# Performance work log

Measured on AMD Instinct MI355X. Metric: run time of the kernel, lower is better.

## Reference

```python
import jax, jax.numpy as jnp
import numpy as np

TEMP = 13.544
EPS = 1e-5  # BatchNorm2d default eps


def setup_inputs() -> dict:
    key = jax.random.key(0)
    k1, = jax.random.split(key, 1)
    N, S, E = 16, 1024, 512
    x = jax.random.normal(k1, (N, S, E), dtype=jnp.float32)
    gamma = jnp.ones((1,), dtype=jnp.float32)   # BatchNorm2d(1).weight
    beta = jnp.zeros((1,), dtype=jnp.float32)   # BatchNorm2d(1).bias
    return {"x": x, "gamma": gamma, "beta": beta}


def reference(x, gamma, beta):
    # Pairwise squared L2 distances via GEMM identity:
    # ||a-b||^2 = ||a||^2 + ||b||^2 - 2 a.b   (symmetric, matches the
    # original broadcast diff+square+sum without the O(S^2 E) intermediate)
    sq = jnp.sum(x * x, axis=-1)                    # (N, S)
    gram = jnp.einsum('bse,bte->bst', x, x)         # (N, S, S)
    d = sq[:, :, None] + sq[:, None, :] - 2.0 * gram  # (N, S, S)
    d = jnp.maximum(d, 0.0)                          # numerical floor (exact math is >= 0)

    # BatchNorm2d(1) in training mode: stats over all elements of the single channel
    d = d[:, None, :, :]                             # (N, 1, S, S)
    mean = jnp.mean(d)
    var = jnp.mean((d - mean) ** 2)                  # biased variance, as torch uses for normalization
    d_hat = (d - mean) * jax.lax.rsqrt(var + EPS)
    out = d_hat * gamma.reshape(1, 1, 1, 1) + beta.reshape(1, 1, 1, 1)

    # softmax(-out / 13.544) over last dim
    return jax.nn.softmax(-out / TEMP, axis=-1)      # (N, 1, S, S)
```

## Files before the change

kernel.cpp:

```cpp
#include <hip/hip_runtime.h>
#include <hip/hip_bf16.h>


#define S_DIM 1024
#define E_DIM 512
#define NBATCH 16
#define NSTEP (E_DIM / 32)
#define TEMP_C 13.544

typedef __attribute__((ext_vector_type(4))) float f32x4;
typedef __attribute__((ext_vector_type(8))) short bf16x8;
typedef __attribute__((ext_vector_type(8))) _Float16 f16x8;

__device__ inline unsigned pkbf(float lo, float hi) {
  unsigned a = __float_as_uint(lo), b = __float_as_uint(hi);
  a = (a + 0x7FFFu + ((a >> 16) & 1u)) >> 16;
  b = (b + 0x7FFFu + ((b >> 16) & 1u)) & 0xFFFF0000u;
  return b | a;
}

__device__ inline void gload16(const void* g, void* l) {
  __builtin_amdgcn_global_load_lds(
      (const __attribute__((address_space(1))) unsigned*)g,
      (__attribute__((address_space(3))) unsigned*)l, 16, 0, 0);
}

__global__ __launch_bounds__(256) void sqcvt(const float* __restrict__ x,
                                             ushort* __restrict__ xb16,
                                             float* __restrict__ sq,
                                             double* __restrict__ sums) {
  const int wave = threadIdx.x >> 6, lane = threadIdx.x & 63;
  const size_t row = (size_t)blockIdx.x * 4 + wave;
  const float4* xr = reinterpret_cast<const float4*>(x + row * E_DIM);
  float4 a = xr[lane * 2], b = xr[lane * 2 + 1];
  uint4 p;
  p.x = pkbf(a.x, a.y); p.y = pkbf(a.z, a.w);
  p.z = pkbf(b.x, b.y); p.w = pkbf(b.z, b.w);
  *reinterpret_cast<uint4*>(xb16 + row * E_DIM + lane * 8) = p;
  float s = a.x*a.x + a.y*a.y + a.z*a.z + a.w*a.w +
            b.x*b.x + b.y*b.y + b.z*b.z + b.w*b.w;
#pragma unroll
  for (int o = 32; o > 0; o >>= 1) s += __shfl_xor(s, o);
  if (lane == 0) sq[row] = s;
  if (blockIdx.x == 0 && threadIdx.x == 0) { sums[0] = 0.0; sums[1] = 0.0; }
}

template <int MODE>
__global__ __launch_bounds__(256) void gram4(const ushort* __restrict__ xb16,
                                             const float* __restrict__ sq,
                                             float* __restrict__ dout,
                                             _Float16* __restrict__ dp,
                                             double* __restrict__ sums) {
  __shared__ ushort lA[3][4096];
  __shared__ ushort lB[3][4096];
  __shared__ double red[8];

  const int tid = threadIdx.x, wave = tid >> 6, lane = tid & 63;
  const int wr = wave >> 1, wc = wave & 1;

  const int bid = blockIdx.x;
  const int xcd = bid & 7, li = bid >> 3;
  const int b = (xcd << 1) | (li >> 6);
  const int tile = li & 63;
  const int tr = tile >> 3, tc = tile & 7;

  const ushort* xb = xb16 + (size_t)b * (S_DIM * E_DIM);
  const int rowA0 = tr * 128, rowB0 = tc * 128;

  int eA[2], eB[2];
  const int o0 = wave * 1024 + lane * 16;
#pragma unroll
  for (int i = 0; i < 2; ++i) {
    int o = o0 + i * 4096;
    int so = o ^ (((o >> 7) & 3) << 4);
    int row = so >> 6, cb = (so >> 4) & 3;
    eA[i] = (rowA0 + row) * E_DIM + cb * 8;
    eB[i] = (rowB0 + row) * E_DIM + cb * 8;
  }

  auto stage = [&](int buf, int k0) {
    char* la = (char*)&lA[buf][0];
    char* lb = (char*)&lB[buf][0];
    gload16(xb + eA[0] + k0, la + wave * 1024);
    gload16(xb + eA[1] + k0, la + 4096 + wave * 1024);
    gload16(xb + eB[0] + k0, lb + wave * 1024);
    gload16(xb + eB[1] + k0, lb + 4096 + wave * 1024);
  };

  f32x4 acc[4][4] = {};

  stage(0, 0);
  stage(1, 32);
  int cur = 0;
#pragma unroll 1
  for (int ks = 0; ks < NSTEP; ++ks) {
    if (ks < NSTEP - 1) {
      asm volatile("s_waitcnt vmcnt(4)" ::: "memory");
    } else {
      asm volatile("s_waitcnt vmcnt(0)" ::: "memory");
    }
    __builtin_amdgcn_s_barrier();
    __builtin_amdgcn_sched_barrier(0);
    if (ks + 2 < NSTEP) {
      int nb = cur + 2; if (nb >= 3) nb -= 3;
      stage(nb, (ks + 2) * 32);
    }
    __builtin_amdgcn_sched_barrier(0);

    bf16x8 af[4], bfr[4];
    const int cb = lane >> 4;
    const char* la = (const char*)&lA[cur][0];
    const char* lb = (const char*)&lB[cur][0];
#pragma unroll
    for (int m = 0; m < 4; ++m) {
      int row = wr * 64 + m * 16 + (lane & 15);
      af[m] = *reinterpret_cast<const bf16x8*>(la + row * 64 + ((cb ^ ((row >> 1) & 3)) << 4));
    }
#pragma unroll
    for (int n = 0; n < 4; ++n) {
      int row = wc * 64 + n * 16 + (lane & 15);
      bfr[n] = *reinterpret_cast<const bf16x8*>(lb + row * 64 + ((cb ^ ((row >> 1) & 3)) << 4));
    }
#pragma unroll
    for (int m = 0; m < 4; ++m)
#pragma unroll
      for (int n = 0; n < 4; ++n)
        acc[m][n] = __builtin_amdgcn_mfma_f32_16x16x32_bf16(af[m], bfr[n], acc[m][n], 0, 0, 0);

    if (++cur >= 3) cur = 0;
  }

  const float* sqb = sq + b * S_DIM;
  double sd = 0.0, sd2 = 0.0;
#pragma unroll
  for (int m = 0; m < 4; ++m) {
    int gr0 = tr * 128 + wr * 64 + m * 16 + ((lane >> 4) << 2);
    float sqr0 = sqb[gr0], sqr1 = sqb[gr0 + 1], sqr2 = sqb[gr0 + 2], sqr3 = sqb[gr0 + 3];
#pragma unroll
    for (int n = 0; n < 4; ++n) {
      int gc = tc * 128 + wc * 64 + n * 16 + (lane & 15);
      float sqc = sqb[gc];
      float d0 = fmaxf(sqr0 + sqc - 2.0f * acc[m][n][0], 0.0f);
      float d1 = fmaxf(sqr1 + sqc - 2.0f * acc[m][n][1], 0.0f);
      float d2 = fmaxf(sqr2 + sqc - 2.0f * acc[m][n][2], 0.0f);
      float d3 = fmaxf(sqr3 + sqc - 2.0f * acc[m][n][3], 0.0f);
      if (MODE == 0) {
        float* dbase = dout + (size_t)b * S_DIM * S_DIM;
        dbase[(size_t)(gr0 + 0) * S_DIM + gc] = d0;
        dbase[(size_t)(gr0 + 1) * S_DIM + gc] = d1;
        dbase[(size_t)(gr0 + 2) * S_DIM + gc] = d2;
        dbase[(size_t)(gr0 + 3) * S_DIM + gc] = d3;
      } else {
        _Float16* dbase = dp + (size_t)b * S_DIM * S_DIM;
        dbase[(size_t)(gr0 + 0) * S_DIM + gc] = (_Float16)(d0 - sqr0);
        dbase[(size_t)(gr0 + 1) * S_DIM + gc] = (_Float16)(d1 - sqr1);
        dbase[(size_t)(gr0 + 2) * S_DIM + gc] = (_Float16)(d2 - sqr2);
        dbase[(size_t)(gr0 + 3) * S_DIM + gc] = (_Float16)(d3 - sqr3);
      }
      sd += (double)d0 + (double)d1 + (double)d2 + (double)d3;
      sd2 += (double)d0 * d0 + (double)d1 * d1 + (double)d2 * d2 + (double)d3 * d3;
    }
  }
#pragma unroll
  for (int o = 32; o > 0; o >>= 1) {
    sd += __shfl_xor(sd, o);
    sd2 += __shfl_xor(sd2, o);
  }
  if (lane == 0) { red[wave] = sd; red[4 + wave] = sd2; }
  __syncthreads();
  if (tid == 0) {
    atomicAdd(&sums[0], red[0] + red[1] + red[2] + red[3]);
    atomicAdd(&sums[1], red[4] + red[5] + red[6] + red[7]);
  }
}

__device__ inline float ln_scale(const double* sums, const float* gamma) {
  constexpr double invN = 1.0 / (16.0 * 1024.0 * 1024.0);
  double mean = sums[0] * invN;
  double var = sums[1] * invN - mean * mean;
  return (float)(-((double)gamma[0]) / (sqrt(var + 1e-5) * TEMP_C));
}

__global__ __launch_bounds__(256) void softmax_f32(float* __restrict__ d,
                                                   const double* __restrict__ sums,
                                                   const float* __restrict__ gamma) {
  const int wave = threadIdx.x >> 6, lane = threadIdx.x & 63;
  const size_t row = (size_t)blockIdx.x * 4 + wave;
  const float scale = ln_scale(sums, gamma);
  float4* r4 = reinterpret_cast<float4*>(d + row * S_DIM);
  float4 v[4];
#pragma unroll
  for (int i = 0; i < 4; ++i) v[i] = r4[lane + 64 * i];
  float l[16];
#pragma unroll
  for (int i = 0; i < 4; ++i) {
    l[4*i+0] = scale * v[i].x; l[4*i+1] = scale * v[i].y;
    l[4*i+2] = scale * v[i].z; l[4*i+3] = scale * v[i].w;
  }
  float mx = l[0];
#pragma unroll
  for (int i = 1; i < 16; ++i) mx = fmaxf(mx, l[i]);
#pragma unroll
  for (int o = 32; o > 0; o >>= 1) mx = fmaxf(mx, __shfl_xor(mx, o));
  const float L2E = 1.4426950408889634f;
  float e[16], s = 0.f;
#pragma unroll
  for (int i = 0; i < 16; ++i) { e[i] = exp2f((l[i] - mx) * L2E); s += e[i]; }
#pragma unroll
  for (int o = 32; o > 0; o >>= 1) s += __shfl_xor(s, o);
  float inv = 1.0f / s;
#pragma unroll
  for (int i = 0; i < 4; ++i)
    r4[lane + 64 * i] = make_float4(e[4*i]*inv, e[4*i+1]*inv, e[4*i+2]*inv, e[4*i+3]*inv);
}

__global__ __launch_bounds__(256) void softmax_f16(const _Float16* __restrict__ dp,
                                                   float* __restrict__ out,
                                                   const double* __restrict__ sums,
                                                   const float* __restrict__ gamma) {
  const int wave = threadIdx.x >> 6, lane = threadIdx.x & 63;
  const size_t row = (size_t)blockIdx.x * 4 + wave;
  const float scale = ln_scale(sums, gamma);
  const f16x8* r8 = reinterpret_cast<const f16x8*>(dp + row * S_DIM);
  f16x8 h0 = r8[lane * 2], h1 = r8[lane * 2 + 1];
  float l[16];
#pragma unroll
  for (int i = 0; i < 8; ++i) { l[i] = scale * (float)h0[i]; l[8 + i] = scale * (float)h1[i]; }
  float mx = l[0];
#pragma unroll
  for (int i = 1; i < 16; ++i) mx = fmaxf(mx, l[i]);
#pragma unroll
  for (int o = 32; o > 0; o >>= 1) mx = fmaxf(mx, __shfl_xor(mx, o));
  const float L2E = 1.4426950408889634f;
  float e[16], s = 0.f;
#pragma unroll
  for (int i = 0; i < 16; ++i) { e[i] = exp2f((l[i] - mx) * L2E); s += e[i]; }
#pragma unroll
  for (int o = 32; o > 0; o >>= 1) s += __shfl_xor(s, o);
  float inv = 1.0f / s;
  float4* o4 = reinterpret_cast<float4*>(out + row * S_DIM);
#pragma unroll
  for (int i = 0; i < 4; ++i)
    o4[lane * 4 + i] = make_float4(e[4*i]*inv, e[4*i+1]*inv, e[4*i+2]*inv, e[4*i+3]*inv);
}

extern "C" void kernel_launch(void* const* d_in, const int* in_sizes, int n_in,
                              void* d_out, int out_size, void* d_ws, size_t ws_size,
                              hipStream_t stream) {
  const float* x = (const float*)d_in[0];
  const float* gamma = (const float*)d_in[1];
  float* out = (float*)d_out;
  double* sums = (double*)d_ws;
  float* sq = (float*)((char*)d_ws + 256);
  ushort* xb16 = (ushort*)((char*)d_ws + 256 + 65536);
  _Float16* dp = (_Float16*)((char*)d_ws + 256 + 65536 +
                             (size_t)NBATCH * S_DIM * E_DIM * 2);
  const size_t need_b = 256 + 65536 + (size_t)NBATCH * S_DIM * E_DIM * 2;
  const size_t need_a = need_b + (size_t)NBATCH * S_DIM * S_DIM * 2;

  sqcvt<<<dim3(NBATCH * S_DIM / 4), dim3(256), 0, stream>>>(x, xb16, sq, sums);
  if (ws_size >= need_a) {
    gram4<1><<<dim3(NBATCH * 64), dim3(256), 0, stream>>>(xb16, sq, out, dp, sums);
    softmax_f16<<<dim3(NBATCH * S_DIM / 4), dim3(256), 0, stream>>>(dp, out, sums, gamma);
  } else {
    gram4<0><<<dim3(NBATCH * 64), dim3(256), 0, stream>>>(xb16, sq, out, dp, sums);
    softmax_f32<<<dim3(NBATCH * S_DIM / 4), dim3(256), 0, stream>>>(out, sums, gamma);
  }
}
```

Before: 158.7 us.

## Enlarge gram tiles to 256x256 with 8-wave blocks

The gram kernel now computes 256x256 output tiles per block using 512 threads (8 waves, 2x4 layout, each wave 128x64), instead of 128x128 tiles with 4 waves. The grid shrinks to 256 blocks, exactly one wave of blocks across the GPU, and each LDS-staged k-slice is reused across more output, which cuts global and LDS traffic per FLOP. In exchange, accumulator register use doubles, the 3-stage LDS buffers double to 96KB per block, and the reduction covers 8 waves.

```diff
diff --git a/kernel.cpp b/kernel.cpp
--- a/kernel.cpp
+++ b/kernel.cpp
@@ -46,48 +46,47 @@
 }
 
 template <int MODE>
-__global__ __launch_bounds__(256) void gram4(const ushort* __restrict__ xb16,
-                                             const float* __restrict__ sq,
-                                             float* __restrict__ dout,
-                                             _Float16* __restrict__ dp,
-                                             double* __restrict__ sums) {
-  __shared__ ushort lA[3][4096];
-  __shared__ ushort lB[3][4096];
-  __shared__ double red[8];
+__global__ __launch_bounds__(512, 2) void gram5(const ushort* __restrict__ xb16,
+                                                const float* __restrict__ sq,
+                                                float* __restrict__ dout,
+                                                _Float16* __restrict__ dp,
+                                                double* __restrict__ sums) {
+  __shared__ ushort lA[3][8192];
+  __shared__ ushort lB[3][8192];
+  __shared__ double red[16];
 
   const int tid = threadIdx.x, wave = tid >> 6, lane = tid & 63;
-  const int wr = wave >> 1, wc = wave & 1;
+  const int wr = wave >> 2, wc = wave & 3;
 
   const int bid = blockIdx.x;
-  const int xcd = bid & 7, li = bid >> 3;
-  const int b = (xcd << 1) | (li >> 6);
-  const int tile = li & 63;
-  const int tr = tile >> 3, tc = tile & 7;
+  const int xcd = bid & 7, j = bid >> 3;
+  const int b = xcd * 2 + (j >> 4);
+  const int tile = j & 15;
+  const int tr = tile >> 2, tc = tile & 3;
 
   const ushort* xb = xb16 + (size_t)b * (S_DIM * E_DIM);
-  const int rowA0 = tr * 128, rowB0 = tc * 128;
+  const int rowA0 = tr * 256, rowB0 = tc * 256;
 
   int eA[2], eB[2];
-  const int o0 = wave * 1024 + lane * 16;
 #pragma unroll
   for (int i = 0; i < 2; ++i) {
-    int o = o0 + i * 4096;
-    int so = o ^ (((o >> 7) & 3) << 4);
-    int row = so >> 6, cb = (so >> 4) & 3;
-    eA[i] = (rowA0 + row) * E_DIM + cb * 8;
-    eB[i] = (rowB0 + row) * E_DIM + cb * 8;
+    int p = i * 512 + tid;
+    int r = p >> 2;
+    int s = (p & 3) ^ ((r >> 1) & 3);
+    eA[i] = (rowA0 + r) * E_DIM + s * 8;
+    eB[i] = (rowB0 + r) * E_DIM + s * 8;
   }
 
   auto stage = [&](int buf, int k0) {
     char* la = (char*)&lA[buf][0];
     char* lb = (char*)&lB[buf][0];
-    gload16(xb + eA[0] + k0, la + wave * 1024);
-    gload16(xb + eA[1] + k0, la + 4096 + wave * 1024);
-    gload16(xb + eB[0] + k0, lb + wave * 1024);
-    gload16(xb + eB[1] + k0, lb + 4096 + wave * 1024);
+    gload16(xb + eA[0] + k0, la + (wave * 64 + lane) * 16);
+    gload16(xb + eA[1] + k0, la + 8192 + (wave * 64 + lane) * 16);
+    gload16(xb + eB[0] + k0, lb + (wave * 64 + lane) * 16);
+    gload16(xb + eB[1] + k0, lb + 8192 + (wave * 64 + lane) * 16);
   };
 
-  f32x4 acc[4][4] = {};
+  f32x4 acc[8][4] = {};
 
   stage(0, 0);
   stage(1, 32);
@@ -107,22 +106,22 @@
     }
     __builtin_amdgcn_sched_barrier(0);
 
-    bf16x8 af[4], bfr[4];
-    const int cb = lane >> 4;
+    bf16x8 af[8], bfr[4];
+    const int s0 = lane >> 4;
     const char* la = (const char*)&lA[cur][0];
     const char* lb = (const char*)&lB[cur][0];
 #pragma unroll
-    for (int m = 0; m < 4; ++m) {
-      int row = wr * 64 + m * 16 + (lane & 15);
-      af[m] = *reinterpret_cast<const bf16x8*>(la + row * 64 + ((cb ^ ((row >> 1) & 3)) << 4));
+    for (int m = 0; m < 8; ++m) {
+      int row = wr * 128 + m * 16 + (lane & 15);
+      af[m] = *reinterpret_cast<const bf16x8*>(la + row * 64 + ((s0 ^ ((row >> 1) & 3)) << 4));
     }
 #pragma unroll
     for (int n = 0; n < 4; ++n) {
       int row = wc * 64 + n * 16 + (lane & 15);
-      bfr[n] = *reinterpret_cast<const bf16x8*>(lb + row * 64 + ((cb ^ ((row >> 1) & 3)) << 4));
-    }
-#pragma unroll
-    for (int m = 0; m < 4; ++m)
+      bfr[n] = *reinterpret_cast<const bf16x8*>(lb + row * 64 + ((s0 ^ ((row >> 1) & 3)) << 4));
+    }
+#pragma unroll
+    for (int m = 0; m < 8; ++m)
 #pragma unroll
       for (int n = 0; n < 4; ++n)
         acc[m][n] = __builtin_amdgcn_mfma_f32_16x16x32_bf16(af[m], bfr[n], acc[m][n], 0, 0, 0);
@@ -133,12 +132,12 @@
   const float* sqb = sq + b * S_DIM;
   double sd = 0.0, sd2 = 0.0;
 #pragma unroll
-  for (int m = 0; m < 4; ++m) {
-    int gr0 = tr * 128 + wr * 64 + m * 16 + ((lane >> 4) << 2);
+  for (int m = 0; m < 8; ++m) {
+    int gr0 = tr * 256 + wr * 128 + m * 16 + ((lane >> 4) << 2);
     float sqr0 = sqb[gr0], sqr1 = sqb[gr0 + 1], sqr2 = sqb[gr0 + 2], sqr3 = sqb[gr0 + 3];
 #pragma unroll
     for (int n = 0; n < 4; ++n) {
-      int gc = tc * 128 + wc * 64 + n * 16 + (lane & 15);
+      int gc = tc * 256 + wc * 64 + n * 16 + (lane & 15);
       float sqc = sqb[gc];
       float d0 = fmaxf(sqr0 + sqc - 2.0f * acc[m][n][0], 0.0f);
       float d1 = fmaxf(sqr1 + sqc - 2.0f * acc[m][n][1], 0.0f);
@@ -166,11 +165,14 @@
     sd += __shfl_xor(sd, o);
     sd2 += __shfl_xor(sd2, o);
   }
-  if (lane == 0) { red[wave] = sd; red[4 + wave] = sd2; }
+  if (lane == 0) { red[wave] = sd; red[8 + wave] = sd2; }
   __syncthreads();
   if (tid == 0) {
-    atomicAdd(&sums[0], red[0] + red[1] + red[2] + red[3]);
-    atomicAdd(&sums[1], red[4] + red[5] + red[6] + red[7]);
+    double t1 = 0.0, t2 = 0.0;
+#pragma unroll
+    for (int w = 0; w < 8; ++w) { t1 += red[w]; t2 += red[8 + w]; }
+    atomicAdd(&sums[0], t1);
+    atomicAdd(&sums[1], t2);
   }
 }
 
@@ -260,10 +262,10 @@
 
   sqcvt<<<dim3(NBATCH * S_DIM / 4), dim3(256), 0, stream>>>(x, xb16, sq, sums);
   if (ws_size >= need_a) {
-    gram4<1><<<dim3(NBATCH * 64), dim3(256), 0, stream>>>(xb16, sq, out, dp, sums);
+    gram5<1><<<dim3(256), dim3(512), 0, stream>>>(xb16, sq, out, dp, sums);
     softmax_f16<<<dim3(NBATCH * S_DIM / 4), dim3(256), 0, stream>>>(dp, out, sums, gamma);
   } else {
-    gram4<0><<<dim3(NBATCH * 64), dim3(256), 0, stream>>>(xb16, sq, out, dp, sums);
+    gram5<0><<<dim3(256), dim3(512), 0, stream>>>(xb16, sq, out, dp, sums);
     softmax_f32<<<dim3(NBATCH * S_DIM / 4), dim3(256), 0, stream>>>(out, sums, gamma);
   }
 }
```

Result: faster. 144.4 us (-9.0%).
